# Performance work log

Hardware: AMD Instinct MI355X
Metric: run time of the kernel (lower is better)

The kernel has to match this reference:

```python
import jax, jax.numpy as jnp
import numpy as np

MARGIN = 0.2
ENCODER_STRIDE = 320


def setup_inputs() -> dict:
    key = jax.random.key(0)
    k1, k2, k3, k4 = jax.random.split(key, 4)
    B, D, T, NC = 8, 512, 2048, 4096
    student_features = jax.random.normal(k1, (B, D, T), dtype=jnp.float32)
    codebook = jax.random.normal(k2, (NC, D), dtype=jnp.float32)
    teacher_codes = jax.random.randint(k3, (B, T), 0, NC, dtype=jnp.int64)
    lengths = jax.random.randint(k4, (B,), 0, T * ENCODER_STRIDE, dtype=jnp.int64)
    return {
        "student_features": student_features,
        "teacher_codes": teacher_codes,
        "codebook": codebook,
        "lengths": lengths,
    }


def reference(student_features, teacher_codes, codebook, lengths):
    B, D, T = student_features.shape
    # frame-level valid mask: (B, T)
    frame_lengths = lengths // ENCODER_STRIDE
    mask = (jnp.arange(T)[None, :] < frame_lengths[:, None]).astype(student_features.dtype)

    # (B*T, D) flattened student vectors
    z = jnp.transpose(student_features, (0, 2, 1)).reshape(-1, D)

    # Euclidean cdist via ||z||^2 + ||c||^2 - 2 z c^T (matmul form, like torch.cdist)
    sq = (
        jnp.sum(z * z, axis=-1, keepdims=True)
        + jnp.sum(codebook * codebook, axis=-1)[None, :]
        - 2.0 * jnp.einsum("nd,cd->nc", z, codebook)
    )
    dists = jnp.sqrt(jnp.maximum(sq, 1e-12))  # (B*T, num_codes)

    teacher_flat = teacher_codes.reshape(-1)
    rows = jnp.arange(teacher_flat.shape[0])
    pos_dist = dists[rows, teacher_flat]
    # exclude the target code, then min over codebook
    dists_for_neg = dists.at[rows, teacher_flat].set(jnp.inf)
    neg_dist = jnp.min(dists_for_neg, axis=1)

    triplet = jax.nn.relu(pos_dist.reshape(B, T) - neg_dist.reshape(B, T) + MARGIN)
    loss = jnp.sum(triplet * mask) / (jnp.sum(mask) + 1e-8)
    return loss
```

## Files before the change

kernel.cpp:

```cpp
#include <hip/hip_runtime.h>
#include <hip/hip_bf16.h>

typedef float f32x4 __attribute__((ext_vector_type(4)));
typedef int v8i __attribute__((ext_vector_type(8)));

#define NB 8
#define ND 512
#define NT 2048
#define NCODES 4096
#define NM (NB * NT)
#define MARGIN_F 0.2f
#define ENC_STRIDE 320


static __device__ inline bool rank_decode(const int* __restrict__ lengths, int rank,
                                          int shift, int& b, int& tib) {
    int acc = 0;
    bool ok = false;
#pragma unroll
    for (int bb = 0; bb < NB; bb++) {
        int fl = lengths[bb] / ENC_STRIDE;
        int c = (fl + ((1 << shift) - 1)) >> shift;
        if (!ok && rank < acc + c) { b = bb; tib = rank - acc; ok = true; }
        acc += c;
    }
    return ok;
}

__global__ void prep_fused(const float* __restrict__ sf, const float* __restrict__ cb,
                           const int* __restrict__ lengths,
                           unsigned char* __restrict__ Zq, float* __restrict__ npart,
                           unsigned char* __restrict__ Cq, float* __restrict__ cnorm,
                           float* __restrict__ accum, unsigned int* __restrict__ ticket) {
    __shared__ float tile[128][65];
    __shared__ float redc[4][16];
    const int tid = threadIdx.x;
    const int wave = tid >> 6, lane = tid & 63, l15 = lane & 15, kq = lane >> 4;

    if (blockIdx.x < 1024) {
        const int bx = blockIdx.x;
        int b, tt;
        if (!rank_decode(lengths, bx >> 2, 6, b, tt)) return;
        const int t0 = tt * 64;
        const int d0 = (bx & 3) * 128;
        const float* src = sf + (size_t)b * ND * NT;
#pragma unroll
        for (int it = 0; it < 8; it++) {
            int idx = it * 256 + tid;
            int d = idx >> 4, t4 = (idx & 15) * 4;
            float4 v = *(const float4*)(src + (size_t)(d0 + d) * NT + t0 + t4);
            tile[d][t4] = v.x; tile[d][t4 + 1] = v.y; tile[d][t4 + 2] = v.z; tile[d][t4 + 3] = v.w;
        }
        __syncthreads();
        const int m0 = b * NT + t0;
        {
            const int trow = wave * 16 + l15;
            unsigned char q[32];
#pragma unroll
            for (int j = 0; j < 32; j += 2) {
                float a = tile[kq * 32 + j][trow];
                float c = tile[kq * 32 + j + 1][trow];
                int p = __builtin_amdgcn_cvt_pk_fp8_f32(a, c, 0, false);
                q[j] = (unsigned char)(p & 0xFF);
                q[j + 1] = (unsigned char)((p >> 8) & 0xFF);
            }
            const int M_ = m0 >> 7, rg = ((m0 >> 4) & 7) + wave, K_ = d0 >> 7;
            char* base = (char*)Zq + ((size_t)((M_ * 4 + K_) * 8 + rg)) * 2048;
            *(uint4*)(base + lane * 16) = *(uint4*)&q[0];
            *(uint4*)(base + 1024 + lane * 16) = *(uint4*)&q[16];
        }
        if (tid < 64) {
            float s = 0.0f;
#pragma unroll 16
            for (int d = 0; d < 128; d++) {
                float v = tile[d][tid];
                s += v * v;
            }
            npart[(size_t)(d0 >> 7) * NM + m0 + tid] = s;
        }
    } else {
        if (blockIdx.x == 1279 && tid == 0) { *accum = 0.0f; *ticket = 0u; }
        const int r0 = (blockIdx.x - 1024) * 16;
        const int row = r0 + l15;
        const int K_ = wave;
        const float* src = cb + (size_t)row * ND + K_ * 128 + kq * 32;
        unsigned char q[32];
        float s = 0.0f;
#pragma unroll
        for (int j4 = 0; j4 < 8; j4++) {
            float4 v = *(const float4*)(src + j4 * 4);
            s += v.x * v.x + v.y * v.y + v.z * v.z + v.w * v.w;
            int p0 = __builtin_amdgcn_cvt_pk_fp8_f32(v.x, v.y, 0, false);
            int p1 = __builtin_amdgcn_cvt_pk_fp8_f32(v.z, v.w, 0, false);
            q[j4 * 4 + 0] = (unsigned char)(p0 & 0xFF);
            q[j4 * 4 + 1] = (unsigned char)((p0 >> 8) & 0xFF);
            q[j4 * 4 + 2] = (unsigned char)(p1 & 0xFF);
            q[j4 * 4 + 3] = (unsigned char)((p1 >> 8) & 0xFF);
        }
        const int N_ = r0 >> 7, rg = (r0 >> 4) & 7;
        char* base = (char*)Cq + ((size_t)((N_ * 4 + K_) * 8 + rg)) * 2048;
        *(uint4*)(base + lane * 16) = *(uint4*)&q[0];
        *(uint4*)(base + 1024 + lane * 16) = *(uint4*)&q[16];
        s += __shfl_xor(s, 16);
        s += __shfl_xor(s, 32);
        if (lane < 16) redc[wave][l15] = s;
        __syncthreads();
        if (tid < 16) cnorm[r0 + tid] = redc[0][tid] + redc[1][tid] + redc[2][tid] + redc[3][tid];
    }
}

static __device__ inline v8i ldfrag(const char* p) {
    union { uint4 q[2]; v8i v; } u;
    u.q[0] = *(const uint4*)p;
    u.q[1] = *(const uint4*)(p + 1024);
    return u.v;
}

__global__ __launch_bounds__(256, 3) void triplet_main(
    const unsigned char* __restrict__ Zq, const unsigned char* __restrict__ Cq,
    const float* __restrict__ cnorm, const int* __restrict__ teacher,
    const int* __restrict__ lengths,
    float* __restrict__ negq, float* __restrict__ posq) {
    __shared__ float smn[2][64], smp[2][64];

    const int blk = (int)blockIdx.x;
    const int x = blk & 7;
    const int rest = blk >> 3;
    const int N_ = rest & 31;
    const int kk = rest >> 5;
    const int m_rank = x + 8 * kk;
    int b, tM;
    if (!rank_decode(lengths, m_rank, 7, b, tM)) return;
    const int M_ = b * 16 + tM;
    const int m0 = M_ * 128;

    const int tid = threadIdx.x;
    const int wave = tid >> 6, lane = tid & 63;
    const int wr = wave >> 1, wc = wave & 1;
    const int l15 = lane & 15, quad = lane >> 4;

    const float INF = __builtin_inff();
    int tch[4][4];
#pragma unroll
    for (int mi = 0; mi < 4; mi++)
#pragma unroll
        for (int r = 0; r < 4; r++)
            tch[mi][r] = teacher[m0 + wr * 64 + mi * 16 + quad * 4 + r];

    const char* gA = (const char*)Zq + (size_t)(M_ * 4) * 16384 +
                     (size_t)(wr * 4) * 2048 + lane * 16;
    const char* gB = (const char*)Cq + (size_t)(N_ * 4) * 16384 +
                     (size_t)(wc * 4) * 2048 + lane * 16;

    f32x4 acc[4][4];
#pragma unroll
    for (int mi = 0; mi < 4; mi++)
#pragma unroll
        for (int ni = 0; ni < 4; ni++)
            acc[mi][ni] = (f32x4){0.f, 0.f, 0.f, 0.f};

#pragma unroll 1
    for (int kt = 0; kt < 4; ++kt) {
        const char* pA = gA + (size_t)kt * 16384;
        const char* pB = gB + (size_t)kt * 16384;
        v8i av[4], bv[4];
#pragma unroll
        for (int mi = 0; mi < 4; mi++) av[mi] = ldfrag(pA + mi * 2048);
#pragma unroll
        for (int ni = 0; ni < 4; ni++) bv[ni] = ldfrag(pB + ni * 2048);
#pragma unroll
        for (int mi = 0; mi < 4; mi++)
#pragma unroll
            for (int ni = 0; ni < 4; ni++)
                acc[mi][ni] = __builtin_amdgcn_mfma_scale_f32_16x16x128_f8f6f4(
                    av[mi], bv[ni], acc[mi][ni], 0, 0,
                    0, 0x7F7F7F7F, 0, 0x7F7F7F7F);
    }

    const int n0 = N_ * 128;
    float cn[4]; int col[4];
#pragma unroll
    for (int ni = 0; ni < 4; ni++) {
        col[ni] = n0 + wc * 64 + ni * 16 + l15;
        cn[ni] = cnorm[col[ni]];
    }
    float rmn[4][4], rps[4][4];
#pragma unroll
    for (int mi = 0; mi < 4; mi++)
#pragma unroll
        for (int r = 0; r < 4; r++) {
            int t = tch[mi][r];
            float mn = INF, ps = INF;
#pragma unroll
            for (int ni = 0; ni < 4; ni++) {
                float val = fmaf(-2.0f, acc[mi][ni][r], cn[ni]);
                bool ist = (col[ni] == t);
                mn = fminf(mn, ist ? INF : val);
                ps = fminf(ps, ist ? val : INF);
            }
#pragma unroll
            for (int off = 1; off < 16; off <<= 1) {
                mn = fminf(mn, __shfl_xor(mn, off));
                ps = fminf(ps, __shfl_xor(ps, off));
            }
            rmn[mi][r] = mn;
            rps[mi][r] = ps;
        }

    if (wc == 1 && l15 == 0) {
#pragma unroll
        for (int mi = 0; mi < 4; mi++)
#pragma unroll
            for (int r = 0; r < 4; r++) {
                smn[wr][mi * 16 + quad * 4 + r] = rmn[mi][r];
                smp[wr][mi * 16 + quad * 4 + r] = rps[mi][r];
            }
    }
    __syncthreads();
    if (wc == 0 && l15 == 0) {
#pragma unroll
        for (int mi = 0; mi < 4; mi++)
#pragma unroll
            for (int r = 0; r < 4; r++) {
                int rl = mi * 16 + quad * 4 + r;
                float mn = fminf(rmn[mi][r], smn[wr][rl]);
                float ps = fminf(rps[mi][r], smp[wr][rl]);
                int m = m0 + wr * 64 + rl;
                negq[(size_t)N_ * NM + m] = mn;
                posq[(size_t)N_ * NM + m] = ps;
            }
    }
}

__global__ void reduce_final(const float* __restrict__ negq, const float* __restrict__ posq,
                             const float* __restrict__ npart, const int* __restrict__ lengths,
                             float* __restrict__ accum, unsigned int* __restrict__ ticket,
                             float* __restrict__ out) {
    const float INF = __builtin_inff();
    const int m = blockIdx.x * 256 + threadIdx.x;
    float mn = INF, ps = INF;
#pragma unroll 8
    for (int s = 0; s < 32; s++) {
        mn = fminf(mn, negq[(size_t)s * NM + m]);
        ps = fminf(ps, posq[(size_t)s * NM + m]);
    }
    float zn = npart[m] + npart[NM + m] + npart[2 * NM + m] + npart[3 * NM + m];
    float negd = sqrtf(fmaxf(zn + mn, 1e-12f));
    float posd = sqrtf(fmaxf(zn + ps, 1e-12f));
    float tri = fmaxf(posd - negd + MARGIN_F, 0.0f);
    int b = m >> 11;
    int tt = m & (NT - 1);
    int flen = lengths[b] / ENC_STRIDE;
    float val = (tt < flen) ? tri : 0.0f;

    __shared__ float red[4];
#pragma unroll
    for (int off = 1; off < 64; off <<= 1) val += __shfl_xor(val, off);
    int lane = threadIdx.x & 63, w = threadIdx.x >> 6;
    if (lane == 0) red[w] = val;
    __syncthreads();
    if (threadIdx.x == 0) {
        atomicAdd(accum, red[0] + red[1] + red[2] + red[3]);
        __threadfence();
        unsigned int old = atomicAdd(ticket, 1u);
        if (old == 63u) {
            float total = atomicAdd(accum, 0.0f);
            float cnt = 0.0f;
            for (int bb = 0; bb < NB; bb++) cnt += (float)(lengths[bb] / ENC_STRIDE);
            out[0] = total / (cnt + 1e-8f);
        }
    }
}

extern "C" void kernel_launch(void* const* d_in, const int* in_sizes, int n_in,
                              void* d_out, int out_size, void* d_ws, size_t ws_size,
                              hipStream_t stream) {
    const float* sf = (const float*)d_in[0];
    const int* teacher = (const int*)d_in[1];
    const float* cb = (const float*)d_in[2];
    const int* lengths = (const int*)d_in[3];

    char* ws = (char*)d_ws;
    unsigned char* Zq = (unsigned char*)(ws);
    unsigned char* Cq = (unsigned char*)(ws + 8388608);
    float* cnorm = (float*)(ws + 10485760);
    float* npart = (float*)(ws + 10502144);
    float* negq = (float*)(ws + 10764288);
    float* posq = (float*)(ws + 12861440);
    float* accum = (float*)(ws + 14958592);
    unsigned int* ticket = (unsigned int*)(ws + 14958596);

    prep_fused<<<1280, 256, 0, stream>>>(sf, cb, lengths, Zq, npart, Cq, cnorm, accum, ticket);
    triplet_main<<<4096, 256, 0, stream>>>(Zq, Cq, cnorm, teacher, lengths, negq, posq);
    reduce_final<<<64, 256, 0, stream>>>(negq, posq, npart, lengths, accum, ticket,
                                         (float*)d_out);
}
```

Measured before the change: 130.0 us.

## Split norm and final reductions across all waves and raise MFMA wave priority

In the prep kernel, the per-row squared norm is now computed by all four waves, each covering 32 feature dims, and combined through shared memory, where before a single wave looped over 128 dims. The final reduction kernel launches 256 blocks of 64 rows with four waves each, and each wave reduces 8 of the 32 column-chunk partial minima before combining them in shared memory. This exposes more parallelism for the small tail kernel. The MFMA loop in the main kernel is wrapped in s_setprio so the matrix issue takes precedence over other waves; the two reduction changes add a barrier and extra atomics respectively.

```diff
diff --git a/kernel.cpp b/kernel.cpp
--- a/kernel.cpp
+++ b/kernel.cpp
@@ -34,6 +34,7 @@
                            float* __restrict__ accum, unsigned int* __restrict__ ticket) {
     __shared__ float tile[128][65];
     __shared__ float redc[4][16];
+    __shared__ float rnp[4][64];
     const int tid = threadIdx.x;
     const int wave = tid >> 6, lane = tid & 63, l15 = lane & 15, kq = lane >> 4;
 
@@ -69,14 +70,19 @@
             *(uint4*)(base + lane * 16) = *(uint4*)&q[0];
             *(uint4*)(base + 1024 + lane * 16) = *(uint4*)&q[16];
         }
-        if (tid < 64) {
+        {
+            const int t = tid & 63, dg = tid >> 6;
             float s = 0.0f;
-#pragma unroll 16
-            for (int d = 0; d < 128; d++) {
-                float v = tile[d][tid];
+#pragma unroll 8
+            for (int d = 0; d < 32; d++) {
+                float v = tile[dg * 32 + d][t];
                 s += v * v;
             }
-            npart[(size_t)(d0 >> 7) * NM + m0 + tid] = s;
+            rnp[dg][t] = s;
+            __syncthreads();
+            if (tid < 64)
+                npart[(size_t)(d0 >> 7) * NM + m0 + tid] =
+                    rnp[0][tid] + rnp[1][tid] + rnp[2][tid] + rnp[3][tid];
         }
     } else {
         if (blockIdx.x == 1279 && tid == 0) { *accum = 0.0f; *ticket = 0u; }
@@ -168,6 +174,7 @@
         for (int mi = 0; mi < 4; mi++) av[mi] = ldfrag(pA + mi * 2048);
 #pragma unroll
         for (int ni = 0; ni < 4; ni++) bv[ni] = ldfrag(pB + ni * 2048);
+        __builtin_amdgcn_s_setprio(1);
 #pragma unroll
         for (int mi = 0; mi < 4; mi++)
 #pragma unroll
@@ -175,6 +182,7 @@
                 acc[mi][ni] = __builtin_amdgcn_mfma_scale_f32_16x16x128_f8f6f4(
                     av[mi], bv[ni], acc[mi][ni], 0, 0,
                     0, 0x7F7F7F7F, 0, 0x7F7F7F7F);
+        __builtin_amdgcn_s_setprio(0);
     }
 
     const int n0 = N_ * 128;
@@ -237,37 +245,42 @@
                              float* __restrict__ accum, unsigned int* __restrict__ ticket,
                              float* __restrict__ out) {
     const float INF = __builtin_inff();
-    const int m = blockIdx.x * 256 + threadIdx.x;
+    const int t = threadIdx.x & 63;
+    const int sg = threadIdx.x >> 6;
+    const int m = blockIdx.x * 64 + t;
     float mn = INF, ps = INF;
-#pragma unroll 8
-    for (int s = 0; s < 32; s++) {
-        mn = fminf(mn, negq[(size_t)s * NM + m]);
-        ps = fminf(ps, posq[(size_t)s * NM + m]);
-    }
-    float zn = npart[m] + npart[NM + m] + npart[2 * NM + m] + npart[3 * NM + m];
-    float negd = sqrtf(fmaxf(zn + mn, 1e-12f));
-    float posd = sqrtf(fmaxf(zn + ps, 1e-12f));
-    float tri = fmaxf(posd - negd + MARGIN_F, 0.0f);
-    int b = m >> 11;
-    int tt = m & (NT - 1);
-    int flen = lengths[b] / ENC_STRIDE;
-    float val = (tt < flen) ? tri : 0.0f;
-
-    __shared__ float red[4];
-#pragma unroll
-    for (int off = 1; off < 64; off <<= 1) val += __shfl_xor(val, off);
-    int lane = threadIdx.x & 63, w = threadIdx.x >> 6;
-    if (lane == 0) red[w] = val;
+#pragma unroll
+    for (int s = 0; s < 8; s++) {
+        mn = fminf(mn, negq[(size_t)(sg * 8 + s) * NM + m]);
+        ps = fminf(ps, posq[(size_t)(sg * 8 + s) * NM + m]);
+    }
+    __shared__ float cmn[4][64], cps[4][64];
+    cmn[sg][t] = mn;
+    cps[sg][t] = ps;
     __syncthreads();
-    if (threadIdx.x == 0) {
-        atomicAdd(accum, red[0] + red[1] + red[2] + red[3]);
-        __threadfence();
-        unsigned int old = atomicAdd(ticket, 1u);
-        if (old == 63u) {
-            float total = atomicAdd(accum, 0.0f);
-            float cnt = 0.0f;
-            for (int bb = 0; bb < NB; bb++) cnt += (float)(lengths[bb] / ENC_STRIDE);
-            out[0] = total / (cnt + 1e-8f);
+    if (sg == 0) {
+        mn = fminf(fminf(cmn[0][t], cmn[1][t]), fminf(cmn[2][t], cmn[3][t]));
+        ps = fminf(fminf(cps[0][t], cps[1][t]), fminf(cps[2][t], cps[3][t]));
+        float zn = npart[m] + npart[NM + m] + npart[2 * NM + m] + npart[3 * NM + m];
+        float negd = sqrtf(fmaxf(zn + mn, 1e-12f));
+        float posd = sqrtf(fmaxf(zn + ps, 1e-12f));
+        float tri = fmaxf(posd - negd + MARGIN_F, 0.0f);
+        int b = m >> 11;
+        int tt = m & (NT - 1);
+        int flen = lengths[b] / ENC_STRIDE;
+        float val = (tt < flen) ? tri : 0.0f;
+#pragma unroll
+        for (int off = 1; off < 64; off <<= 1) val += __shfl_xor(val, off);
+        if (t == 0) {
+            atomicAdd(accum, val);
+            __threadfence();
+            unsigned int old = atomicAdd(ticket, 1u);
+            if (old == 255u) {
+                float total = atomicAdd(accum, 0.0f);
+                float cnt = 0.0f;
+                for (int bb = 0; bb < NB; bb++) cnt += (float)(lengths[bb] / ENC_STRIDE);
+                out[0] = total / (cnt + 1e-8f);
+            }
         }
     }
 }
@@ -292,6 +305,6 @@
 
     prep_fused<<<1280, 256, 0, stream>>>(sf, cb, lengths, Zq, npart, Cq, cnorm, accum, ticket);
     triplet_main<<<4096, 256, 0, stream>>>(Zq, Cq, cnorm, teacher, lengths, negq, posq);
-    reduce_final<<<64, 256, 0, stream>>>(negq, posq, npart, lengths, accum, ticket,
-                                         (float*)d_out);
-}
+    reduce_final<<<256, 256, 0, stream>>>(negq, posq, npart, lengths, accum, ticket,
+                                          (float*)d_out);
+}
```

Result: no change. 130.8 us (+0.7%).
